# Kernel tuning notes

Measured on AMD Instinct MI355X. Metric: run time of the kernel, lower is better.

## Reference

```python
import jax, jax.numpy as jnp
import numpy as np

B, S, D, H, E, K = 4, 2048, 512, 2048, 8, 2


def setup_inputs() -> dict:
    key = jax.random.key(0)
    k0, k1, k2, k3 = jax.random.split(key, 4)
    return {
        "x": jax.random.normal(k0, (B, S, D), jnp.float32),
        "router_w": jax.random.normal(k1, (E, D), jnp.float32) * 0.02,
        "router_b": jnp.zeros((E,), jnp.float32),
        "w1": jax.random.normal(k2, (E, D, H), jnp.float32) * 0.02,
        "b1": jnp.zeros((E, H), jnp.float32),
        "w2": jax.random.normal(k3, (E, H, D), jnp.float32) * 0.02,
        "b2": jnp.zeros((E, D), jnp.float32),
        "top_k": K,
    }


def reference(x, router_w, router_b, w1, b1, w2, b2, top_k):
    # x: [B, S, D]; eval mode (no router noise, no dropout)
    Bb, Ss, Dd = x.shape
    Ee = w1.shape[0]
    xf = x.reshape(-1, Dd)                                   # [T, D], T = B*S
    router_logits = xf @ router_w.T + router_b               # [T, E]
    top_v, top_i = jax.lax.top_k(router_logits, top_k)       # [T, K]
    rw = jax.nn.softmax(top_v, axis=-1)                      # [T, K]
    # combine[t, e] = sum_k rw[t, k] * (top_i[t, k] == e); zero for unrouted experts
    combine = jnp.sum(jax.nn.one_hot(top_i, Ee, dtype=xf.dtype) * rw[..., None], axis=1)  # [T, E]
    out = jnp.zeros_like(xf)
    for e in range(Ee):  # fixed small expert count; each iter is a dense GEMM pair
        h = jax.nn.gelu(xf @ w1[e] + b1[e], approximate=False)  # exact erf GELU like torch nn.GELU
        y = h @ w2[e] + b2[e]                                   # [T, D]
        out = out + combine[:, e:e + 1] * y
    return out.reshape(Bb, Ss, Dd), router_logits
```

## Files before the change

kernel.cpp:

```cpp
#include <hip/hip_runtime.h>
#include <hip/hip_bf16.h>

#define TTOK 8192
#define DDIM 512
#define HDIM 2048
#define NEXP 8
#define RBLK 256
#define RTOK (TTOK / RBLK)

typedef __bf16 bf16x8 __attribute__((ext_vector_type(8)));
typedef float f32x4 __attribute__((ext_vector_type(4)));
typedef unsigned short us8 __attribute__((ext_vector_type(8)));

__device__ __forceinline__ unsigned short f2bf(float f) {
  unsigned int u = __builtin_bit_cast(unsigned int, f);
  u += 0x7fffu + ((u >> 16) & 1u);
  return (unsigned short)(u >> 16);
}

__device__ __forceinline__ void gll16(const void* g, void* l) {
  __builtin_amdgcn_global_load_lds(
      (__attribute__((address_space(1))) void*)g,
      (__attribute__((address_space(3))) void*)l, 16, 0, 0);
}

__global__ __launch_bounds__(256) void k_router(
    const float* __restrict__ x, const float* __restrict__ rw,
    const float* __restrict__ rb, float* __restrict__ logits,
    unsigned short* __restrict__ xb,
    short* __restrict__ texp, unsigned short* __restrict__ tpos,
    float* __restrict__ tgate, int* __restrict__ blockcnt) {
  __shared__ int lcnt[NEXP];
  const int tid = threadIdx.x, wid = tid >> 6, lane = tid & 63;
  if (tid < NEXP) lcnt[tid] = 0;
  __syncthreads();
  float4 w0[NEXP], w1[NEXP];
  float rbv[NEXP];
#pragma unroll
  for (int e = 0; e < NEXP; ++e) {
    const float4* wp = (const float4*)(rw + e * DDIM);
    w0[e] = wp[lane * 2];
    w1[e] = wp[lane * 2 + 1];
    rbv[e] = rb[e];
  }
  const int tbase = blockIdx.x * RTOK;
  for (int it = 0; it < RTOK / 4; ++it) {
    const int t = tbase + it * 4 + wid;
    const float4* xr = (const float4*)(x + (size_t)t * DDIM);
    float4 v0 = xr[lane * 2], v1 = xr[lane * 2 + 1];
    us8 o;
    o[0] = f2bf(v0.x); o[1] = f2bf(v0.y); o[2] = f2bf(v0.z); o[3] = f2bf(v0.w);
    o[4] = f2bf(v1.x); o[5] = f2bf(v1.y); o[6] = f2bf(v1.z); o[7] = f2bf(v1.w);
    *(us8*)(xb + (size_t)t * DDIM + lane * 8) = o;
    float a[NEXP];
#pragma unroll
    for (int e = 0; e < NEXP; ++e)
      a[e] = v0.x * w0[e].x + v0.y * w0[e].y + v0.z * w0[e].z + v0.w * w0[e].w +
             v1.x * w1[e].x + v1.y * w1[e].y + v1.z * w1[e].z + v1.w * w1[e].w;
#pragma unroll
    for (int off = 32; off > 0; off >>= 1)
#pragma unroll
      for (int e = 0; e < NEXP; ++e) a[e] += __shfl_xor(a[e], off, 64);
    if (lane == 0) {
      float lg[NEXP];
#pragma unroll
      for (int e = 0; e < NEXP; ++e) lg[e] = a[e] + rbv[e];
      float4 s0, s1;
      s0.x = lg[0]; s0.y = lg[1]; s0.z = lg[2]; s0.w = lg[3];
      s1.x = lg[4]; s1.y = lg[5]; s1.z = lg[6]; s1.w = lg[7];
      ((float4*)(logits + t * NEXP))[0] = s0;
      ((float4*)(logits + t * NEXP))[1] = s1;
      int i0 = 0; float m0 = lg[0];
#pragma unroll
      for (int e = 1; e < NEXP; ++e) if (lg[e] > m0) { m0 = lg[e]; i0 = e; }
      int i1 = 0; float m1 = -3.4e38f;
#pragma unroll
      for (int e = 0; e < NEXP; ++e) if (e != i0 && lg[e] > m1) { m1 = lg[e]; i1 = e; }
      float e1 = expf(m1 - m0);
      float inv = 1.0f / (1.0f + e1);
      int p0 = atomicAdd(&lcnt[i0], 1);
      int p1 = atomicAdd(&lcnt[i1], 1);
      texp[t * 2] = (short)i0;     tpos[t * 2] = (unsigned short)p0;     tgate[t * 2] = inv;
      texp[t * 2 + 1] = (short)i1; tpos[t * 2 + 1] = (unsigned short)p1; tgate[t * 2 + 1] = e1 * inv;
    }
  }
  __syncthreads();
  if (tid < NEXP) blockcnt[blockIdx.x * NEXP + tid] = lcnt[tid];
}

__global__ void k_offsets(const int* __restrict__ blockcnt, int* __restrict__ blockbase,
                          int* __restrict__ counts, int* __restrict__ offsets) {
  const int e = threadIdx.x;
  if (e < NEXP) {
    int run = 0;
#pragma unroll 8
    for (int b = 0; b < RBLK; ++b) {
      blockbase[b * NEXP + e] = run;
      run += blockcnt[b * NEXP + e];
    }
    counts[e] = run;
  }
  __syncthreads();
  if (e == 0) {
    int s = 0;
    for (int q = 0; q < NEXP; ++q) { offsets[q] = s; s += counts[q]; }
  }
}

__global__ void k_scatter(const short* __restrict__ texp, const unsigned short* __restrict__ tpos,
                          const float* __restrict__ tgate, const int* __restrict__ blockbase,
                          const int* __restrict__ offsets,
                          int* __restrict__ toklist, int* __restrict__ cidx,
                          float* __restrict__ cgate) {
  const int t = blockIdx.x * 256 + threadIdx.x;
  const int b = t / RTOK;
#pragma unroll
  for (int k = 0; k < 2; ++k) {
    const int e = (int)texp[t * 2 + k];
    const int pos = blockbase[b * NEXP + e] + (int)tpos[t * 2 + k];
    toklist[e * TTOK + pos] = t;
    cidx[t * 2 + k] = offsets[e] + pos;
    cgate[t * 2 + k] = tgate[t * 2 + k];
  }
}

__global__ void k_transpose2(const float* __restrict__ w1, const float* __restrict__ w2,
                             unsigned short* __restrict__ w1t, unsigned short* __restrict__ w2t) {
  __shared__ float tile[32][33];
  const int id = blockIdx.x;
  const float* in; unsigned short* out; int R, C, rem;
  if (id < 8192) {
    const int e = id >> 10; rem = id & 1023;
    R = DDIM; C = HDIM;
    in = w1 + (size_t)e * R * C; out = w1t + (size_t)e * R * C;
  } else {
    const int e = (id - 8192) >> 10; rem = (id - 8192) & 1023;
    R = HDIM; C = DDIM;
    in = w2 + (size_t)e * R * C; out = w2t + (size_t)e * R * C;
  }
  const int ctiles = C >> 5;
  const int c0 = (rem % ctiles) * 32, r0 = (rem / ctiles) * 32;
  const int tx = threadIdx.x, ty = threadIdx.y;
#pragma unroll
  for (int i = 0; i < 32; i += 8)
    tile[ty + i][tx] = in[(size_t)(r0 + ty + i) * C + (c0 + tx)];
  __syncthreads();
#pragma unroll
  for (int i = 0; i < 32; i += 8)
    out[(size_t)(c0 + ty + i) * R + (r0 + tx)] = f2bf(tile[tx][ty + i]);
}

template <int PHASE>
__global__ __launch_bounds__(512, 4) void k_gemm(
    const unsigned short* __restrict__ A, const unsigned short* __restrict__ Bt,
    const float* __restrict__ bias, const int* __restrict__ counts,
    const int* __restrict__ offsets, const int* __restrict__ toklist,
    unsigned short* __restrict__ Out) {
  constexpr int K = (PHASE == 1) ? DDIM : HDIM;
  constexpr int NN = (PHASE == 1) ? HDIM : DDIM;
  constexpr int KB = K * 2;
  constexpr int NX = NN / 128;
  constexpr int NXSH = (PHASE == 1) ? 4 : 2;
  constexpr int NT = K / 64;

  const int id = blockIdx.x;
  const int e = id & 7;
  const int p = id >> 3;
  const int cnt = counts[e];
  const int m0 = (p >> NXSH) * 128;
  if (m0 >= cnt) return;
  const int n0 = (p & (NX - 1)) * 128;
  const int off = offsets[e];

  __shared__ alignas(16) unsigned char smem[2][32768];

  const int tid = threadIdx.x;
  const int wid = tid >> 6, lane = tid & 63;

  const char* src[4];
  unsigned dst[4];
#pragma unroll
  for (int i = 0; i < 4; ++i) {
    const int c = i * 8 + wid;
    const bool isA = c < 16;
    const int cc = isA ? c : c - 16;
    const int r = cc * 8 + (lane >> 3);
    const int cs = ((lane & 7) * 16) ^ ((r & 7) << 4);
    if (isA) {
      int mrow = m0 + r; if (mrow > cnt - 1) mrow = cnt - 1;
      if (PHASE == 1) {
        const int tok = toklist[(e << 13) + mrow];
        src[i] = (const char*)A + (size_t)tok * (DDIM * 2) + cs;
      } else {
        src[i] = (const char*)A + (size_t)(off + mrow) * KB + cs;
      }
    } else {
      src[i] = (const char*)Bt + (size_t)e * NN * KB + (size_t)(n0 + r) * KB + cs;
    }
    dst[i] = (isA ? 0u : 16384u) + cc * 1024;
  }

  f32x4 acc[4][2] = {};

  const int wr = wid >> 2, wc = wid & 3;
  const int lr = lane & 15, lk = lane >> 4;

#pragma unroll
  for (int i = 0; i < 4; ++i) gll16(src[i], &smem[0][0] + dst[i]);
  __syncthreads();

  int cur = 0;
  for (int t = 0; t < NT; ++t) {
    if (t + 1 < NT) {
      const int kb = (t + 1) * 128;
#pragma unroll
      for (int i = 0; i < 4; ++i) gll16(src[i] + kb, &smem[cur ^ 1][0] + dst[i]);
    }
    const unsigned cb = (unsigned)cur * 32768u;
#pragma unroll
    for (int kk = 0; kk < 2; ++kk) {
      bf16x8 af[4], bv[2];
#pragma unroll
      for (int mi = 0; mi < 4; ++mi) {
        const int r = wr * 64 + mi * 16 + lr;
        const unsigned byteo = cb + r * 128 + ((kk * 64 + lk * 16) ^ ((r & 7) << 4));
        af[mi] = *(const bf16x8*)(&smem[0][0] + byteo);
      }
#pragma unroll
      for (int ni = 0; ni < 2; ++ni) {
        const int r = wc * 32 + ni * 16 + lr;
        const unsigned byteo = cb + 16384 + r * 128 + ((kk * 64 + lk * 16) ^ ((r & 7) << 4));
        bv[ni] = *(const bf16x8*)(&smem[0][0] + byteo);
      }
#pragma unroll
      for (int mi = 0; mi < 4; ++mi)
#pragma unroll
        for (int ni = 0; ni < 2; ++ni)
          acc[mi][ni] = __builtin_amdgcn_mfma_f32_16x16x32_bf16(af[mi], bv[ni], acc[mi][ni], 0, 0, 0);
    }
    if (t + 1 < NT) __syncthreads();
    cur ^= 1;
  }

  const int lq = lane >> 4;
#pragma unroll
  for (int mi = 0; mi < 4; ++mi) {
#pragma unroll
    for (int ni = 0; ni < 2; ++ni) {
      const int n = n0 + wc * 32 + ni * 16 + lr;
      const float bv_ = bias[e * NN + n];
#pragma unroll
      for (int r2 = 0; r2 < 4; ++r2) {
        const int m = m0 + wr * 64 + mi * 16 + lq * 4 + r2;
        if (m < cnt) {
          if (PHASE == 1) {
            const float xv = acc[mi][ni][r2] + bv_;
            const float u = xv * (0.7978845608f + 0.0356774081f * xv * xv);
            const float g = xv / (1.0f + __expf(-2.0f * u));
            Out[(size_t)(off + m) * HDIM + n] = f2bf(g);
          } else {
            Out[(size_t)(off + m) * DDIM + n] = f2bf(acc[mi][ni][r2] + bv_);
          }
        }
      }
    }
  }
}

__global__ __launch_bounds__(256) void k_combine(const unsigned short* __restrict__ yp,
                                                 const int* __restrict__ cidx,
                                                 const float* __restrict__ cgate,
                                                 float* __restrict__ out) {
  const int t = blockIdx.x * 4 + (threadIdx.x >> 6);
  const int lane = threadIdx.x & 63;
  const int i0 = cidx[t * 2], i1 = cidx[t * 2 + 1];
  const float g0 = cgate[t * 2], g1 = cgate[t * 2 + 1];
  us8 a = *(const us8*)(yp + (size_t)i0 * DDIM + lane * 8);
  us8 b = *(const us8*)(yp + (size_t)i1 * DDIM + lane * 8);
  float o[8];
#pragma unroll
  for (int j = 0; j < 8; ++j) {
    const float va = __builtin_bit_cast(float, (unsigned)a[j] << 16);
    const float vb = __builtin_bit_cast(float, (unsigned)b[j] << 16);
    o[j] = g0 * va + g1 * vb;
  }
  float* op = out + (size_t)t * DDIM + lane * 8;
  *(float4*)op = *(float4*)o;
  *(float4*)(op + 4) = *(float4*)(o + 4);
}

extern "C" void kernel_launch(void* const* d_in, const int* in_sizes, int n_in,
                              void* d_out, int out_size, void* d_ws, size_t ws_size,
                              hipStream_t stream) {
  (void)in_sizes; (void)n_in; (void)out_size; (void)ws_size;
  const float* x  = (const float*)d_in[0];
  const float* rw = (const float*)d_in[1];
  const float* rb = (const float*)d_in[2];
  const float* w1 = (const float*)d_in[3];
  const float* b1 = (const float*)d_in[4];
  const float* w2 = (const float*)d_in[5];
  const float* b2 = (const float*)d_in[6];
  float* out = (float*)d_out;
  float* logits = out + (size_t)TTOK * DDIM;

  char* ws = (char*)d_ws;
  unsigned short* xb  = (unsigned short*)(ws + 0);
  unsigned short* w1t = (unsigned short*)(ws + 8388608);
  unsigned short* w2t = (unsigned short*)(ws + 25165824);
  unsigned short* h   = (unsigned short*)(ws + 41943040);
  int*   toklist = (int*)(ws + 109051904);
  int*   cidx    = (int*)(ws + 109314048);
  float* cgate   = (float*)(ws + 109379584);
  int*   counts  = (int*)(ws + 109445120);
  int*   offsets = (int*)(ws + 109445152);
  unsigned short* yp = w1t;
  char* rsc = ws + 41943040;
  short*          texp      = (short*)(rsc + 0);
  unsigned short* tpos      = (unsigned short*)(rsc + 32768);
  float*          tgate     = (float*)(rsc + 65536);
  int*            blockcnt  = (int*)(rsc + 131072);
  int*            blockbase = (int*)(rsc + 139264);

  k_router<<<RBLK, 256, 0, stream>>>(x, rw, rb, logits, xb, texp, tpos, tgate, blockcnt);
  k_transpose2<<<16384, dim3(32, 8), 0, stream>>>(w1, w2, w1t, w2t);
  k_offsets<<<1, 64, 0, stream>>>(blockcnt, blockbase, counts, offsets);
  k_scatter<<<TTOK / 256, 256, 0, stream>>>(texp, tpos, tgate, blockbase, offsets,
                                            toklist, cidx, cgate);

  k_gemm<1><<<(HDIM / 128) * (TTOK / 128) * NEXP, 512, 0, stream>>>(
      xb, w1t, b1, counts, offsets, toklist, h);
  k_gemm<2><<<(DDIM / 128) * (TTOK / 128) * NEXP, 512, 0, stream>>>(
      h, w2t, b2, counts, offsets, nullptr, yp);
  k_combine<<<TTOK / 4, 256, 0, stream>>>(yp, cidx, cgate, out);
}
```

Baseline: 280.7 us.

## Fuse offsets prefix scan into scatter kernel and unroll GEMM main loop by two

Removes the single-block k_offsets launch by having every scatter block recompute the per-expert prefix sums over the 256 router-block counts and keep its own eight block bases and expert offsets in shared memory. Separately, the GEMM K-loop is unrolled by two with precomputed LDS offsets for both double buffers, so the runtime buffer index and per-iteration address arithmetic go away. The trade is redundant prefix work in each scatter block (a serial 256-step loop per expert) and higher register use from the offset tables, which could affect occupancy at 512 threads with 4 blocks per CU.

```diff
diff --git a/kernel.cpp b/kernel.cpp
--- a/kernel.cpp
+++ b/kernel.cpp
@@ -88,38 +88,42 @@
   if (tid < NEXP) blockcnt[blockIdx.x * NEXP + tid] = lcnt[tid];
 }
 
-__global__ void k_offsets(const int* __restrict__ blockcnt, int* __restrict__ blockbase,
-                          int* __restrict__ counts, int* __restrict__ offsets) {
-  const int e = threadIdx.x;
-  if (e < NEXP) {
+__global__ __launch_bounds__(256) void k_scatter(
+    const short* __restrict__ texp, const unsigned short* __restrict__ tpos,
+    const float* __restrict__ tgate, const int* __restrict__ blockcnt,
+    int* __restrict__ toklist, int* __restrict__ cidx, float* __restrict__ cgate,
+    int* __restrict__ counts, int* __restrict__ offsets) {
+  __shared__ int base[8][NEXP];
+  __shared__ int cnt_sh[NEXP];
+  __shared__ int offs_sh[NEXP];
+  const int tid = threadIdx.x;
+  const int b0 = blockIdx.x * 8;
+  if (tid < NEXP) {
     int run = 0;
 #pragma unroll 8
     for (int b = 0; b < RBLK; ++b) {
-      blockbase[b * NEXP + e] = run;
-      run += blockcnt[b * NEXP + e];
-    }
-    counts[e] = run;
-  }
-  __syncthreads();
-  if (e == 0) {
+      if ((unsigned)(b - b0) < 8u) base[b - b0][tid] = run;
+      run += blockcnt[b * NEXP + tid];
+    }
+    cnt_sh[tid] = run;
+    counts[tid] = run;
+  }
+  __syncthreads();
+  if (tid < NEXP) {
     int s = 0;
-    for (int q = 0; q < NEXP; ++q) { offsets[q] = s; s += counts[q]; }
-  }
-}
-
-__global__ void k_scatter(const short* __restrict__ texp, const unsigned short* __restrict__ tpos,
-                          const float* __restrict__ tgate, const int* __restrict__ blockbase,
-                          const int* __restrict__ offsets,
-                          int* __restrict__ toklist, int* __restrict__ cidx,
-                          float* __restrict__ cgate) {
-  const int t = blockIdx.x * 256 + threadIdx.x;
-  const int b = t / RTOK;
+    for (int q = 0; q < tid; ++q) s += cnt_sh[q];
+    offs_sh[tid] = s;
+    offsets[tid] = s;
+  }
+  __syncthreads();
+  const int t = blockIdx.x * 256 + tid;
+  const int rb = (t / RTOK) - b0;
 #pragma unroll
   for (int k = 0; k < 2; ++k) {
     const int e = (int)texp[t * 2 + k];
-    const int pos = blockbase[b * NEXP + e] + (int)tpos[t * 2 + k];
+    const int pos = base[rb][e] + (int)tpos[t * 2 + k];
     toklist[e * TTOK + pos] = t;
-    cidx[t * 2 + k] = offsets[e] + pos;
+    cidx[t * 2 + k] = offs_sh[e] + pos;
     cgate[t * 2 + k] = tgate[t * 2 + k];
   }
 }
@@ -150,6 +154,26 @@
     out[(size_t)(c0 + ty + i) * R + (r0 + tx)] = f2bf(tile[tx][ty + i]);
 }
 
+template <int B>
+__device__ __forceinline__ void mm_step(const unsigned char* smbase,
+                                        const unsigned (&aoff)[2][2][4],
+                                        const unsigned (&boff)[2][2][2],
+                                        f32x4 (&acc)[4][2]) {
+#pragma unroll
+  for (int kk = 0; kk < 2; ++kk) {
+    bf16x8 af[4], bv[2];
+#pragma unroll
+    for (int mi = 0; mi < 4; ++mi) af[mi] = *(const bf16x8*)(smbase + aoff[B][kk][mi]);
+#pragma unroll
+    for (int ni = 0; ni < 2; ++ni) bv[ni] = *(const bf16x8*)(smbase + boff[B][kk][ni]);
+#pragma unroll
+    for (int mi = 0; mi < 4; ++mi)
+#pragma unroll
+      for (int ni = 0; ni < 2; ++ni)
+        acc[mi][ni] = __builtin_amdgcn_mfma_f32_16x16x32_bf16(af[mi], bv[ni], acc[mi][ni], 0, 0, 0);
+  }
+}
+
 template <int PHASE>
 __global__ __launch_bounds__(512, 4) void k_gemm(
     const unsigned short* __restrict__ A, const unsigned short* __restrict__ Bt,
@@ -173,6 +197,7 @@
   const int off = offsets[e];
 
   __shared__ alignas(16) unsigned char smem[2][32768];
+  unsigned char* smbase = &smem[0][0];
 
   const int tid = threadIdx.x;
   const int wid = tid >> 6, lane = tid & 63;
@@ -200,46 +225,45 @@
     dst[i] = (isA ? 0u : 16384u) + cc * 1024;
   }
 
-  f32x4 acc[4][2] = {};
-
   const int wr = wid >> 2, wc = wid & 3;
   const int lr = lane & 15, lk = lane >> 4;
 
-#pragma unroll
-  for (int i = 0; i < 4; ++i) gll16(src[i], &smem[0][0] + dst[i]);
-  __syncthreads();
-
-  int cur = 0;
-  for (int t = 0; t < NT; ++t) {
-    if (t + 1 < NT) {
-      const int kb = (t + 1) * 128;
-#pragma unroll
-      for (int i = 0; i < 4; ++i) gll16(src[i] + kb, &smem[cur ^ 1][0] + dst[i]);
-    }
-    const unsigned cb = (unsigned)cur * 32768u;
+  unsigned aoff[2][2][4], boff[2][2][2];
+#pragma unroll
+  for (int b = 0; b < 2; ++b)
 #pragma unroll
     for (int kk = 0; kk < 2; ++kk) {
-      bf16x8 af[4], bv[2];
 #pragma unroll
       for (int mi = 0; mi < 4; ++mi) {
         const int r = wr * 64 + mi * 16 + lr;
-        const unsigned byteo = cb + r * 128 + ((kk * 64 + lk * 16) ^ ((r & 7) << 4));
-        af[mi] = *(const bf16x8*)(&smem[0][0] + byteo);
+        aoff[b][kk][mi] = b * 32768u + r * 128 + ((kk * 64 + lk * 16) ^ ((r & 7) << 4));
       }
 #pragma unroll
       for (int ni = 0; ni < 2; ++ni) {
         const int r = wc * 32 + ni * 16 + lr;
-        const unsigned byteo = cb + 16384 + r * 128 + ((kk * 64 + lk * 16) ^ ((r & 7) << 4));
-        bv[ni] = *(const bf16x8*)(&smem[0][0] + byteo);
+        boff[b][kk][ni] = b * 32768u + 16384u + r * 128 + ((kk * 64 + lk * 16) ^ ((r & 7) << 4));
       }
-#pragma unroll
-      for (int mi = 0; mi < 4; ++mi)
-#pragma unroll
-        for (int ni = 0; ni < 2; ++ni)
-          acc[mi][ni] = __builtin_amdgcn_mfma_f32_16x16x32_bf16(af[mi], bv[ni], acc[mi][ni], 0, 0, 0);
-    }
-    if (t + 1 < NT) __syncthreads();
-    cur ^= 1;
+    }
+
+  f32x4 acc[4][2] = {};
+
+#pragma unroll
+  for (int i = 0; i < 4; ++i) gll16(src[i], smbase + dst[i]);
+  __syncthreads();
+
+  for (int t = 0; t < NT; t += 2) {
+#pragma unroll
+    for (int i = 0; i < 4; ++i) gll16(src[i] + 128, smbase + 32768u + dst[i]);
+    mm_step<0>(smbase, aoff, boff, acc);
+    __syncthreads();
+    if (t + 2 < NT) {
+#pragma unroll
+      for (int i = 0; i < 4; ++i) gll16(src[i] + 256, smbase + dst[i]);
+    }
+    mm_step<1>(smbase, aoff, boff, acc);
+    if (t + 2 < NT) __syncthreads();
+#pragma unroll
+    for (int i = 0; i < 4; ++i) src[i] += 256;
   }
 
   const int lq = lane >> 4;
@@ -319,13 +343,11 @@
   unsigned short* tpos      = (unsigned short*)(rsc + 32768);
   float*          tgate     = (float*)(rsc + 65536);
   int*            blockcnt  = (int*)(rsc + 131072);
-  int*            blockbase = (int*)(rsc + 139264);
 
   k_router<<<RBLK, 256, 0, stream>>>(x, rw, rb, logits, xb, texp, tpos, tgate, blockcnt);
   k_transpose2<<<16384, dim3(32, 8), 0, stream>>>(w1, w2, w1t, w2t);
-  k_offsets<<<1, 64, 0, stream>>>(blockcnt, blockbase, counts, offsets);
-  k_scatter<<<TTOK / 256, 256, 0, stream>>>(texp, tpos, tgate, blockbase, offsets,
-                                            toklist, cidx, cgate);
+  k_scatter<<<TTOK / 256, 256, 0, stream>>>(texp, tpos, tgate, blockcnt,
+                                            toklist, cidx, cgate, counts, offsets);
 
   k_gemm<1><<<(HDIM / 128) * (TTOK / 128) * NEXP, 512, 0, stream>>>(
       xb, w1t, b1, counts, offsets, toklist, h);
```

After: 308.7 us. 1.1x slower.

## Rework GEMM k-loop pipelining with explicit vmcnt waits and parallelize offsets scan

Applied to the files above, without the earlier changes.

The GEMM main loop now keeps two stages of global-to-LDS loads in flight. It waits with explicit s_waitcnt vmcnt counts and raw s_barrier instead of __syncthreads, and precomputes the LDS fragment offsets. The aim is to overlap loads for tile t+2 with compute on tile t and to cut barrier and wait overhead. Separately, the serial per-expert offsets loop becomes a wave-level shuffle scan using 512 threads. The hand-tuned waitcnt and barrier placement risks races if the compiler reorders memory operations.

```diff
diff --git a/kernel.cpp b/kernel.cpp
--- a/kernel.cpp
+++ b/kernel.cpp
@@ -88,22 +88,32 @@
   if (tid < NEXP) blockcnt[blockIdx.x * NEXP + tid] = lcnt[tid];
 }
 
-__global__ void k_offsets(const int* __restrict__ blockcnt, int* __restrict__ blockbase,
-                          int* __restrict__ counts, int* __restrict__ offsets) {
-  const int e = threadIdx.x;
-  if (e < NEXP) {
-    int run = 0;
-#pragma unroll 8
-    for (int b = 0; b < RBLK; ++b) {
-      blockbase[b * NEXP + e] = run;
-      run += blockcnt[b * NEXP + e];
-    }
-    counts[e] = run;
-  }
+__global__ __launch_bounds__(512) void k_offsets(const int* __restrict__ blockcnt,
+                                                 int* __restrict__ blockbase,
+                                                 int* __restrict__ counts,
+                                                 int* __restrict__ offsets) {
+  __shared__ int csh[NEXP];
+  const int e = threadIdx.x >> 6, lane = threadIdx.x & 63;
+  int carry = 0;
+#pragma unroll
+  for (int c = 0; c < RBLK; c += 64) {
+    int v = blockcnt[(c + lane) * NEXP + e];
+    int s = v;
+#pragma unroll
+    for (int o = 1; o < 64; o <<= 1) {
+      int u = __shfl_up(s, o, 64);
+      if (lane >= o) s += u;
+    }
+    blockbase[(c + lane) * NEXP + e] = carry + s - v;
+    carry += __shfl(s, 63, 64);
+  }
+  if (lane == 0) csh[e] = carry;
   __syncthreads();
-  if (e == 0) {
+  if (threadIdx.x < NEXP) {
     int s = 0;
-    for (int q = 0; q < NEXP; ++q) { offsets[q] = s; s += counts[q]; }
+    for (int q = 0; q < (int)threadIdx.x; ++q) s += csh[q];
+    offsets[threadIdx.x] = s;
+    counts[threadIdx.x] = csh[threadIdx.x];
   }
 }
 
@@ -150,6 +160,26 @@
     out[(size_t)(c0 + ty + i) * R + (r0 + tx)] = f2bf(tile[tx][ty + i]);
 }
 
+template <int B>
+__device__ __forceinline__ void mm_step(const unsigned char* smbase,
+                                        const unsigned (&aoff)[2][2][4],
+                                        const unsigned (&boff)[2][2][2],
+                                        f32x4 (&acc)[4][2]) {
+#pragma unroll
+  for (int kk = 0; kk < 2; ++kk) {
+    bf16x8 af[4], bv[2];
+#pragma unroll
+    for (int mi = 0; mi < 4; ++mi) af[mi] = *(const bf16x8*)(smbase + aoff[B][kk][mi]);
+#pragma unroll
+    for (int ni = 0; ni < 2; ++ni) bv[ni] = *(const bf16x8*)(smbase + boff[B][kk][ni]);
+#pragma unroll
+    for (int mi = 0; mi < 4; ++mi)
+#pragma unroll
+      for (int ni = 0; ni < 2; ++ni)
+        acc[mi][ni] = __builtin_amdgcn_mfma_f32_16x16x32_bf16(af[mi], bv[ni], acc[mi][ni], 0, 0, 0);
+  }
+}
+
 template <int PHASE>
 __global__ __launch_bounds__(512, 4) void k_gemm(
     const unsigned short* __restrict__ A, const unsigned short* __restrict__ Bt,
@@ -173,6 +203,7 @@
   const int off = offsets[e];
 
   __shared__ alignas(16) unsigned char smem[2][32768];
+  unsigned char* smbase = &smem[0][0];
 
   const int tid = threadIdx.x;
   const int wid = tid >> 6, lane = tid & 63;
@@ -200,46 +231,48 @@
     dst[i] = (isA ? 0u : 16384u) + cc * 1024;
   }
 
-  f32x4 acc[4][2] = {};
-
   const int wr = wid >> 2, wc = wid & 3;
   const int lr = lane & 15, lk = lane >> 4;
 
-#pragma unroll
-  for (int i = 0; i < 4; ++i) gll16(src[i], &smem[0][0] + dst[i]);
-  __syncthreads();
-
-  int cur = 0;
-  for (int t = 0; t < NT; ++t) {
-    if (t + 1 < NT) {
-      const int kb = (t + 1) * 128;
-#pragma unroll
-      for (int i = 0; i < 4; ++i) gll16(src[i] + kb, &smem[cur ^ 1][0] + dst[i]);
-    }
-    const unsigned cb = (unsigned)cur * 32768u;
+  unsigned aoff[2][2][4], boff[2][2][2];
+#pragma unroll
+  for (int b = 0; b < 2; ++b)
 #pragma unroll
     for (int kk = 0; kk < 2; ++kk) {
-      bf16x8 af[4], bv[2];
 #pragma unroll
       for (int mi = 0; mi < 4; ++mi) {
         const int r = wr * 64 + mi * 16 + lr;
-        const unsigned byteo = cb + r * 128 + ((kk * 64 + lk * 16) ^ ((r & 7) << 4));
-        af[mi] = *(const bf16x8*)(&smem[0][0] + byteo);
+        aoff[b][kk][mi] = b * 32768u + r * 128 + ((kk * 64 + lk * 16) ^ ((r & 7) << 4));
       }
 #pragma unroll
       for (int ni = 0; ni < 2; ++ni) {
         const int r = wc * 32 + ni * 16 + lr;
-        const unsigned byteo = cb + 16384 + r * 128 + ((kk * 64 + lk * 16) ^ ((r & 7) << 4));
-        bv[ni] = *(const bf16x8*)(&smem[0][0] + byteo);
+        boff[b][kk][ni] = b * 32768u + 16384u + r * 128 + ((kk * 64 + lk * 16) ^ ((r & 7) << 4));
       }
-#pragma unroll
-      for (int mi = 0; mi < 4; ++mi)
-#pragma unroll
-        for (int ni = 0; ni < 2; ++ni)
-          acc[mi][ni] = __builtin_amdgcn_mfma_f32_16x16x32_bf16(af[mi], bv[ni], acc[mi][ni], 0, 0, 0);
-    }
-    if (t + 1 < NT) __syncthreads();
-    cur ^= 1;
+    }
+
+  f32x4 acc[4][2] = {};
+
+#pragma unroll
+  for (int i = 0; i < 4; ++i) gll16(src[i], smbase + dst[i]);
+#pragma unroll
+  for (int i = 0; i < 4; ++i) gll16(src[i] + 128, smbase + 32768u + dst[i]);
+
+  for (int t = 0; t < NT; ++t) {
+    if (t + 1 < NT) asm volatile("s_waitcnt vmcnt(4)" ::: "memory");
+    else            asm volatile("s_waitcnt vmcnt(0)" ::: "memory");
+    __builtin_amdgcn_s_barrier();
+    __builtin_amdgcn_sched_barrier(0);
+    if (t & 1) mm_step<1>(smbase, aoff, boff, acc);
+    else       mm_step<0>(smbase, aoff, boff, acc);
+    if (t + 2 < NT) {
+      __builtin_amdgcn_s_barrier();
+      __builtin_amdgcn_sched_barrier(0);
+      const int kb = (t + 2) * 128;
+      const unsigned bb = (t & 1) ? 32768u : 0u;
+#pragma unroll
+      for (int i = 0; i < 4; ++i) gll16(src[i] + kb, smbase + bb + dst[i]);
+    }
   }
 
   const int lq = lane >> 4;
@@ -323,7 +356,7 @@
 
   k_router<<<RBLK, 256, 0, stream>>>(x, rw, rb, logits, xb, texp, tpos, tgate, blockcnt);
   k_transpose2<<<16384, dim3(32, 8), 0, stream>>>(w1, w2, w1t, w2t);
-  k_offsets<<<1, 64, 0, stream>>>(blockcnt, blockbase, counts, offsets);
+  k_offsets<<<1, 512, 0, stream>>>(blockcnt, blockbase, counts, offsets);
   k_scatter<<<TTOK / 256, 256, 0, stream>>>(texp, tpos, tgate, blockbase, offsets,
                                             toklist, cidx, cgate);
 
```

Result: no change. 282.2 us (+0.5%).
